# Performance work log

Hardware: AMD Instinct MI355X
Metric: run time of the kernel (lower is better)

## Reference

```python
import jax, jax.numpy as jnp
import numpy as np

MARGIN = 0.2
EPS = 1e-8
N, D_EMB, N_CLASSES = 8192, 256, 512


def setup_inputs() -> dict:
    key = jax.random.key(0)
    k1, k2 = jax.random.split(key)
    embeddings = jax.random.normal(k1, (N, D_EMB), dtype=jnp.float32)
    labels = jax.random.randint(k2, (N,), 0, N_CLASSES, dtype=jnp.int64)
    return {"embeddings": embeddings, "labels": labels}


def reference(embeddings, labels):
    # OnlineTripleLoss.forward with sampling_strategy='fixed_semi_hard', cosine metric.
    n = embeddings.shape[0]
    norms = jnp.linalg.norm(embeddings, axis=1, keepdims=True)
    xn = embeddings / jnp.maximum(norms, EPS)
    dist = 1.0 - xn @ xn.T                       # [N, N] cosine distance

    same = labels[:, None] == labels[None, :]    # same-label mask
    neg_mask = ~same
    has_neg = jnp.any(neg_mask, axis=1)          # anchor has at least one negative

    # fixed_semi_hard argmax(ap+margin-an) == argmin(an); fallback is also argmin(an)
    BIG = jnp.float32(1e9)
    dmin_neg = jnp.min(jnp.where(neg_mask, dist, BIG), axis=1)  # [N]

    # all anchor-positive combinations: same label, a < p (itertools.combinations order)
    upper = jnp.triu(jnp.ones((n, n), dtype=bool), 1)
    pair_mask = same & upper & has_neg[:, None]

    losses = jnp.maximum(dist - dmin_neg[:, None] + MARGIN, 0.0)
    count = jnp.sum(pair_mask)
    loss_sum = jnp.sum(jnp.where(pair_mask, losses, 0.0))
    loss = jnp.where(count > 0, loss_sum / jnp.maximum(count, 1).astype(jnp.float32), 0.0)
    return loss, count
```

## Files before the change

### kernel.cpp

```cpp
#include <hip/hip_runtime.h>
#include <hip/hip_bf16.h>

#define NROWS 8192
#define DEMB 256
#define MARGIN 0.2f
#define NCLS 512
#define TPC 8
#define NSTEP 16
#define MCAP 64
#define SROW 264

typedef __attribute__((ext_vector_type(4))) float f32x4;
typedef __attribute__((ext_vector_type(8))) short bf16x8;

static __device__ __forceinline__ unsigned short f2b(float f) {
    unsigned u = __builtin_bit_cast(unsigned, f);
    u += 0x7fffu + ((u >> 16) & 1u);
    return (unsigned short)(u >> 16);
}
static __device__ __forceinline__ float b2f(unsigned short b) {
    unsigned u = ((unsigned)b) << 16;
    return __builtin_bit_cast(float, u);
}
static __device__ __forceinline__ unsigned encf(float f) {
    unsigned u = __builtin_bit_cast(unsigned, f);
    return (u & 0x80000000u) ? ~u : (u | 0x80000000u);
}
static __device__ __forceinline__ float decf(unsigned e) {
    unsigned u = (e & 0x80000000u) ? (e ^ 0x80000000u) : ~e;
    return __builtin_bit_cast(float, u);
}
static __device__ __forceinline__ void gload16(const void* g, void* l) {
    __builtin_amdgcn_global_load_lds(
        (const __attribute__((address_space(1))) unsigned int*)g,
        (__attribute__((address_space(3))) unsigned int*)l, 16, 0, 0);
}

__global__ __launch_bounds__(256) void k_norm(const float* __restrict__ x,
                                              unsigned short* __restrict__ xnb,
                                              unsigned* __restrict__ amax,
                                              int* __restrict__ bcnt) {
    int gid = blockIdx.x * blockDim.x + threadIdx.x;
    if (gid < NROWS) amax[gid] = 0u;
    if (gid < NCLS) bcnt[gid] = 0;
    int row  = gid >> 6;
    int lane = threadIdx.x & 63;
    const float4* p = reinterpret_cast<const float4*>(x + (size_t)row * DEMB) + lane;
    float4 v = *p;
    float s = v.x * v.x + v.y * v.y + v.z * v.z + v.w * v.w;
#pragma unroll
    for (int m = 1; m < 64; m <<= 1) s += __shfl_xor(s, m);
    float inv = 1.0f / fmaxf(sqrtf(s), 1e-8f);
    ushort4 o;
    o.x = f2b(v.x * inv); o.y = f2b(v.y * inv);
    o.z = f2b(v.z * inv); o.w = f2b(v.w * inv);
    *(reinterpret_cast<ushort4*>(xnb + (size_t)row * DEMB) + lane) = o;
}

__global__ __launch_bounds__(256) void k_bucket(const int* __restrict__ labels,
                                                int* __restrict__ bcnt,
                                                int* __restrict__ mem) {
    int i = blockIdx.x * 256 + threadIdx.x;
    if (i < NROWS) {
        int l = labels[i];
        int slot = atomicAdd(&bcnt[l], 1);
        if (slot < MCAP) mem[l * MCAP + slot] = i;
    }
}

__global__ __launch_bounds__(512, 2) void k_maxneg(const unsigned short* __restrict__ xnb,
                                                   const int* __restrict__ labels,
                                                   unsigned* __restrict__ amax) {
    extern __shared__ char lds[];
    unsigned short* Bl = (unsigned short*)lds;

    int tid  = threadIdx.x;
    int wid  = tid >> 6, lane = tid & 63;
    int wr   = wid >> 1, wc = wid & 1;
    int arow = lane & 15, kgrp = lane >> 4;

    int i0 = blockIdx.x * 128;
    int j0 = blockIdx.y * (TPC * 128);

    bf16x8 a[2][8];
    const unsigned short* ap0 = xnb + (size_t)(i0 + wr * 32 + arow) * DEMB + kgrp * 8;
#pragma unroll
    for (int m = 0; m < 2; ++m)
#pragma unroll
        for (int kk = 0; kk < 8; ++kk)
            a[m][kk] = *(const bf16x8*)(ap0 + m * 16 * DEMB + kk * 32);

    int rlab[2][4];
#pragma unroll
    for (int m = 0; m < 2; ++m)
#pragma unroll
        for (int r = 0; r < 4; ++r)
            rlab[m][r] = labels[i0 + wr * 32 + m * 16 + kgrp * 4 + r];

    float rmax[2][4] = {{-1e30f, -1e30f, -1e30f, -1e30f},
                        {-1e30f, -1e30f, -1e30f, -1e30f}};
    f32x4 acc[2][4] = {};

    auto stage = [&](int buf, int t, int h) {
#pragma unroll
        for (int is = 0; is < 4; ++is) {
            int idx  = is * 512 + tid;
            int row  = idx >> 4;
            int colb = (idx & 15) << 4;
            int scol = (colb ^ ((row & 15) << 4)) >> 1;
            const unsigned short* src =
                xnb + (size_t)(j0 + t * 128 + row) * DEMB + h * 128 + scol;
            unsigned short* dst = Bl + buf * 16384 + is * 4096 + wid * 512;
            gload16(src, dst);
        }
    };

    int clab[4], nlab[4];
    stage(0, 0, 0);
#pragma unroll
    for (int n = 0; n < 4; ++n) clab[n] = labels[j0 + wc * 64 + n * 16 + arow];

    int sw = arow << 4;
    for (int s = 0; s < NSTEP; ++s) {
        __syncthreads();
        if (s + 1 < NSTEP) stage((s + 1) & 1, (s + 1) >> 1, (s + 1) & 1);
        int tile = s >> 1, h = s & 1;
        if (h == 0 && tile + 1 < TPC) {
#pragma unroll
            for (int n = 0; n < 4; ++n)
                nlab[n] = labels[j0 + (tile + 1) * 128 + wc * 64 + n * 16 + arow];
        }
        const char* Bt = (const char*)(Bl + (s & 1) * 16384);
        bf16x8 b[4][4];
#pragma unroll
        for (int n = 0; n < 4; ++n) {
            int rb = (wc * 64 + n * 16 + arow) * 256;
#pragma unroll
            for (int ksl = 0; ksl < 4; ++ksl)
                b[n][ksl] = *(const bf16x8*)(Bt + rb + ((ksl * 64 + kgrp * 16) ^ sw));
        }
#pragma unroll
        for (int m = 0; m < 2; ++m)
#pragma unroll
            for (int n = 0; n < 4; ++n)
#pragma unroll
                for (int ksl = 0; ksl < 4; ++ksl)
                    acc[m][n] = __builtin_amdgcn_mfma_f32_16x16x32_bf16(
                        a[m][h * 4 + ksl], b[n][ksl], acc[m][n], 0, 0, 0);
        if (h == 1) {
#pragma unroll
            for (int m = 0; m < 2; ++m)
#pragma unroll
                for (int r = 0; r < 4; ++r) {
                    float v = rmax[m][r];
                    int rl = rlab[m][r];
#pragma unroll
                    for (int n = 0; n < 4; ++n)
                        if (clab[n] != rl) v = fmaxf(v, acc[m][n][r]);
                    rmax[m][r] = v;
                }
#pragma unroll
            for (int m = 0; m < 2; ++m)
#pragma unroll
                for (int n = 0; n < 4; ++n) acc[m][n] = (f32x4){0.f, 0.f, 0.f, 0.f};
#pragma unroll
            for (int n = 0; n < 4; ++n) clab[n] = nlab[n];
        }
    }

    float* smax = (float*)Bl;
#pragma unroll
    for (int m = 0; m < 2; ++m)
#pragma unroll
        for (int r = 0; r < 4; ++r) {
            float v = rmax[m][r];
#pragma unroll
            for (int msk = 1; msk < 16; msk <<= 1) v = fmaxf(v, __shfl_xor(v, msk));
            if (arow == 0) smax[wc * 128 + wr * 32 + m * 16 + kgrp * 4 + r] = v;
        }
    __syncthreads();
    if (tid < 128) {
        float v = fmaxf(smax[tid], smax[128 + tid]);
        if (v > -1e29f) atomicMax(amax + i0 + tid, encf(v));
    }
}

__global__ __launch_bounds__(256) void k_cpairs2(const unsigned short* __restrict__ xnb,
                                                 const unsigned* __restrict__ amax,
                                                 const int* __restrict__ bcnt,
                                                 const int* __restrict__ mem,
                                                 float* __restrict__ closs,
                                                 int* __restrict__ ccnt) {
    __shared__ unsigned short srows[MCAP * SROW];
    __shared__ int mlist[MCAP];
    __shared__ float sdm[MCAP];
    __shared__ unsigned char shn[MCAP];
    __shared__ float slloss[16];
    __shared__ int slcnt[16];

    int c   = blockIdx.x;
    int tid = threadIdx.x;
    int nc  = bcnt[c];
    if (nc > MCAP) nc = MCAP;

    if (tid < nc) {
        int gi = mem[c * MCAP + tid];
        mlist[tid] = gi;
        unsigned e = amax[gi];
        shn[tid] = (e != 0u);
        sdm[tid] = 1.0f - decf(e);
    }
    __syncthreads();
    int nch = nc * 32;
    for (int ch = tid; ch < nch; ch += 256) {
        int r = ch >> 5, cc = ch & 31;
        *(bf16x8*)(srows + r * SROW + cc * 8) =
            *(const bf16x8*)(xnb + (size_t)mlist[r] * DEMB + cc * 8);
    }
    __syncthreads();

    int slot = tid >> 4, gl = tid & 15;
    int npairs = nc * (nc - 1) / 2;
    float gloss = 0.f;
    int gcnt = 0;
    for (int p = slot; p < npairs; p += 16) {
        int i = 0, rem = p;
        while (rem >= nc - 1 - i) { rem -= nc - 1 - i; ++i; }
        int j = i + 1 + rem;
        bf16x8 a0 = *(const bf16x8*)(srows + i * SROW + gl * 16);
        bf16x8 a1 = *(const bf16x8*)(srows + i * SROW + gl * 16 + 8);
        bf16x8 b0 = *(const bf16x8*)(srows + j * SROW + gl * 16);
        bf16x8 b1 = *(const bf16x8*)(srows + j * SROW + gl * 16 + 8);
        float dot = 0.f;
#pragma unroll
        for (int e = 0; e < 8; ++e) {
            dot += b2f((unsigned short)a0[e]) * b2f((unsigned short)b0[e]);
            dot += b2f((unsigned short)a1[e]) * b2f((unsigned short)b1[e]);
        }
#pragma unroll
        for (int msk = 1; msk < 16; msk <<= 1) dot += __shfl_xor(dot, msk);
        if (gl == 0) {
            int ai = (mlist[i] < mlist[j]) ? i : j;
            if (shn[ai]) {
                gloss += fmaxf(1.0f - dot - sdm[ai] + MARGIN, 0.0f);
                gcnt += 1;
            }
        }
    }
    if (gl == 0) { slloss[slot] = gloss; slcnt[slot] = gcnt; }
    __syncthreads();
    if (tid == 0) {
        float s = 0.f; int k = 0;
        for (int q = 0; q < 16; ++q) { s += slloss[q]; k += slcnt[q]; }
        closs[c] = s; ccnt[c] = k;
    }
}

__global__ __launch_bounds__(256) void k_final(const float* __restrict__ closs,
                                               const int* __restrict__ ccnt,
                                               float* __restrict__ out) {
    __shared__ float sl[256];
    __shared__ int   sc[256];
    int tid = threadIdx.x;
    float s = closs[tid] + closs[tid + 256];
    int   k = ccnt[tid] + ccnt[tid + 256];
    sl[tid] = s; sc[tid] = k;
    __syncthreads();
    for (int st = 128; st > 0; st >>= 1) {
        if (tid < st) {
            sl[tid] += sl[tid + st];
            sc[tid] += sc[tid + st];
        }
        __syncthreads();
    }
    if (tid == 0) {
        out[0] = (sc[0] > 0) ? sl[0] / (float)sc[0] : 0.0f;
        out[1] = (float)sc[0];
    }
}

extern "C" void kernel_launch(void* const* d_in, const int* in_sizes, int n_in,
                              void* d_out, int out_size, void* d_ws, size_t ws_size,
                              hipStream_t stream) {
    const float* emb  = (const float*)d_in[0];
    const int* labels = (const int*)d_in[1];
    float* out = (float*)d_out;

    char* ws = (char*)d_ws;
    unsigned short* xnb = (unsigned short*)ws;
    unsigned* amax = (unsigned*)(ws + (size_t)4 * 1024 * 1024);
    int* bcnt = (int*)(ws + (size_t)4 * 1024 * 1024 + 32768);
    int* mem  = (int*)(ws + (size_t)4 * 1024 * 1024 + 34816);
    float* closs = (float*)(ws + (size_t)4 * 1024 * 1024 + 34816 + 131072);
    int*   ccnt  = (int*)  (ws + (size_t)4 * 1024 * 1024 + 34816 + 131072 + 2048);

    k_norm<<<NROWS / 4, 256, 0, stream>>>(emb, xnb, amax, bcnt);
    k_bucket<<<NROWS / 256, 256, 0, stream>>>(labels, bcnt, mem);
    dim3 g2(NROWS / 128, NCLS / 64);
    k_maxneg<<<g2, 512, 65536, stream>>>(xnb, labels, amax);
    k_cpairs2<<<NCLS, 256, 0, stream>>>(xnb, amax, bcnt, mem, closs, ccnt);
    k_final<<<1, 256, 0, stream>>>(closs, ccnt, out);
}
```

Before: 80.13 us.

## Deepen maxneg LDS pipeline, fuse bucketing into norm, fold final reduce into pairs

The max-negative GEMM kernel now stages 64-wide K slices into a 4-deep ring buffer, using explicit vmcnt waits and raw barriers, MFMA priority boosts and a lighter XOR swizzle. This is meant to hide global-load latency better, and launch bounds now ask for higher occupancy. Label bucketing moves into the normalization kernel, and the separate final reduction kernel is replaced by global atomics with a last-block-done finalize, cutting two launches. The trade-offs are a memset launch, atomic contention, and the risk that the 64KB LDS allocation blocks the requested occupancy.

```diff
diff --git a/kernel.cpp b/kernel.cpp
--- a/kernel.cpp
+++ b/kernel.cpp
@@ -6,7 +6,7 @@
 #define MARGIN 0.2f
 #define NCLS 512
 #define TPC 8
-#define NSTEP 16
+#define NSTEP 32
 #define MCAP 64
 #define SROW 264
 
@@ -37,12 +37,18 @@
 }
 
 __global__ __launch_bounds__(256) void k_norm(const float* __restrict__ x,
+                                              const int* __restrict__ labels,
                                               unsigned short* __restrict__ xnb,
                                               unsigned* __restrict__ amax,
-                                              int* __restrict__ bcnt) {
+                                              int* __restrict__ bcnt,
+                                              int* __restrict__ mem) {
     int gid = blockIdx.x * blockDim.x + threadIdx.x;
-    if (gid < NROWS) amax[gid] = 0u;
-    if (gid < NCLS) bcnt[gid] = 0;
+    if (gid < NROWS) {
+        amax[gid] = 0u;
+        int l = labels[gid];
+        int slot = atomicAdd(&bcnt[l], 1);
+        if (slot < MCAP) mem[l * MCAP + slot] = gid;
+    }
     int row  = gid >> 6;
     int lane = threadIdx.x & 63;
     const float4* p = reinterpret_cast<const float4*>(x + (size_t)row * DEMB) + lane;
@@ -57,22 +63,12 @@
     *(reinterpret_cast<ushort4*>(xnb + (size_t)row * DEMB) + lane) = o;
 }
 
-__global__ __launch_bounds__(256) void k_bucket(const int* __restrict__ labels,
-                                                int* __restrict__ bcnt,
-                                                int* __restrict__ mem) {
-    int i = blockIdx.x * 256 + threadIdx.x;
-    if (i < NROWS) {
-        int l = labels[i];
-        int slot = atomicAdd(&bcnt[l], 1);
-        if (slot < MCAP) mem[l * MCAP + slot] = i;
-    }
-}
-
-__global__ __launch_bounds__(512, 2) void k_maxneg(const unsigned short* __restrict__ xnb,
+__global__ __launch_bounds__(512, 4) void k_maxneg(const unsigned short* __restrict__ xnb,
                                                    const int* __restrict__ labels,
                                                    unsigned* __restrict__ amax) {
     extern __shared__ char lds[];
     unsigned short* Bl = (unsigned short*)lds;
+    const char* BlC = (const char*)lds;
 
     int tid  = threadIdx.x;
     int wid  = tid >> 6, lane = tid & 63;
@@ -97,57 +93,70 @@
         for (int r = 0; r < 4; ++r)
             rlab[m][r] = labels[i0 + wr * 32 + m * 16 + kgrp * 4 + r];
 
+    int row0  = tid >> 3;
+    int colb0 = (tid & 7) << 4;
+    int scol0 = (colb0 ^ ((row0 & 7) << 4)) >> 1;
+    const unsigned short* sb = xnb + (size_t)(j0 + row0) * DEMB + scol0;
+    unsigned short* db = Bl + wid * 512;
+
+    int sx  = (arow & 7) << 4;
+    int rb0 = (wc * 64 + arow) * 128;
+    int rc0 = rb0 + ((kgrp * 16) ^ sx);
+    int rc1 = rb0 + ((64 + kgrp * 16) ^ sx);
+
     float rmax[2][4] = {{-1e30f, -1e30f, -1e30f, -1e30f},
                         {-1e30f, -1e30f, -1e30f, -1e30f}};
     f32x4 acc[2][4] = {};
-
-    auto stage = [&](int buf, int t, int h) {
-#pragma unroll
-        for (int is = 0; is < 4; ++is) {
-            int idx  = is * 512 + tid;
-            int row  = idx >> 4;
-            int colb = (idx & 15) << 4;
-            int scol = (colb ^ ((row & 15) << 4)) >> 1;
-            const unsigned short* src =
-                xnb + (size_t)(j0 + t * 128 + row) * DEMB + h * 128 + scol;
-            unsigned short* dst = Bl + buf * 16384 + is * 4096 + wid * 512;
-            gload16(src, dst);
-        }
-    };
-
     int clab[4], nlab[4];
-    stage(0, 0, 0);
 #pragma unroll
     for (int n = 0; n < 4; ++n) clab[n] = labels[j0 + wc * 64 + n * 16 + arow];
 
-    int sw = arow << 4;
+#define STAGE(S) { \
+        const unsigned short* s_ = sb + ((S) >> 2) * 32768 + ((S) & 3) * 64; \
+        unsigned short* d_ = db + ((S) & 3) * 8192; \
+        gload16(s_, d_); \
+        gload16(s_ + 16384, d_ + 4096); }
+
+    STAGE(0) STAGE(1) STAGE(2)
+
+#pragma unroll
     for (int s = 0; s < NSTEP; ++s) {
-        __syncthreads();
-        if (s + 1 < NSTEP) stage((s + 1) & 1, (s + 1) >> 1, (s + 1) & 1);
-        int tile = s >> 1, h = s & 1;
-        if (h == 0 && tile + 1 < TPC) {
+        if (s + 3 < NSTEP) STAGE(s + 3)
+        if ((s & 3) == 0 && (s >> 2) + 1 < TPC) {
 #pragma unroll
             for (int n = 0; n < 4; ++n)
-                nlab[n] = labels[j0 + (tile + 1) * 128 + wc * 64 + n * 16 + arow];
-        }
-        const char* Bt = (const char*)(Bl + (s & 1) * 16384);
-        bf16x8 b[4][4];
-#pragma unroll
-        for (int n = 0; n < 4; ++n) {
-            int rb = (wc * 64 + n * 16 + arow) * 256;
-#pragma unroll
-            for (int ksl = 0; ksl < 4; ++ksl)
-                b[n][ksl] = *(const bf16x8*)(Bt + rb + ((ksl * 64 + kgrp * 16) ^ sw));
-        }
-#pragma unroll
-        for (int m = 0; m < 2; ++m)
-#pragma unroll
-            for (int n = 0; n < 4; ++n)
-#pragma unroll
-                for (int ksl = 0; ksl < 4; ++ksl)
+                nlab[n] = labels[j0 + ((s >> 2) + 1) * 128 + wc * 64 + n * 16 + arow];
+        }
+        if (s < NSTEP - 3)      asm volatile("s_waitcnt vmcnt(6)" ::: "memory");
+        else if (s == NSTEP - 3) asm volatile("s_waitcnt vmcnt(4)" ::: "memory");
+        else if (s == NSTEP - 2) asm volatile("s_waitcnt vmcnt(2)" ::: "memory");
+        else                     asm volatile("s_waitcnt vmcnt(0)" ::: "memory");
+        __builtin_amdgcn_sched_barrier(0);
+        __builtin_amdgcn_s_barrier();
+        __builtin_amdgcn_sched_barrier(0);
+        {
+            const char* Bt = BlC + (s & 3) * 16384;
+            bf16x8 b[4][2];
+#pragma unroll
+            for (int n = 0; n < 4; ++n) {
+                b[n][0] = *(const bf16x8*)(Bt + n * 2048 + rc0);
+                b[n][1] = *(const bf16x8*)(Bt + n * 2048 + rc1);
+            }
+            __builtin_amdgcn_s_setprio(1);
+#pragma unroll
+            for (int m = 0; m < 2; ++m)
+#pragma unroll
+                for (int n = 0; n < 4; ++n) {
                     acc[m][n] = __builtin_amdgcn_mfma_f32_16x16x32_bf16(
-                        a[m][h * 4 + ksl], b[n][ksl], acc[m][n], 0, 0, 0);
-        if (h == 1) {
+                        a[m][(s & 3) * 2], b[n][0], acc[m][n], 0, 0, 0);
+                    acc[m][n] = __builtin_amdgcn_mfma_f32_16x16x32_bf16(
+                        a[m][(s & 3) * 2 + 1], b[n][1], acc[m][n], 0, 0, 0);
+                }
+            __builtin_amdgcn_s_setprio(0);
+        }
+        __builtin_amdgcn_sched_barrier(0);
+        __builtin_amdgcn_s_barrier();
+        if ((s & 3) == 3) {
 #pragma unroll
             for (int m = 0; m < 2; ++m)
 #pragma unroll
@@ -167,6 +176,7 @@
             for (int n = 0; n < 4; ++n) clab[n] = nlab[n];
         }
     }
+#undef STAGE
 
     float* smax = (float*)Bl;
 #pragma unroll
@@ -189,8 +199,10 @@
                                                  const unsigned* __restrict__ amax,
                                                  const int* __restrict__ bcnt,
                                                  const int* __restrict__ mem,
-                                                 float* __restrict__ closs,
-                                                 int* __restrict__ ccnt) {
+                                                 float* __restrict__ gsum,
+                                                 int* __restrict__ gcnt,
+                                                 unsigned* __restrict__ done,
+                                                 float* __restrict__ out) {
     __shared__ unsigned short srows[MCAP * SROW];
     __shared__ int mlist[MCAP];
     __shared__ float sdm[MCAP];
@@ -222,7 +234,7 @@
     int slot = tid >> 4, gl = tid & 15;
     int npairs = nc * (nc - 1) / 2;
     float gloss = 0.f;
-    int gcnt = 0;
+    int gc = 0;
     for (int p = slot; p < npairs; p += 16) {
         int i = 0, rem = p;
         while (rem >= nc - 1 - i) { rem -= nc - 1 - i; ++i; }
@@ -243,39 +255,25 @@
             int ai = (mlist[i] < mlist[j]) ? i : j;
             if (shn[ai]) {
                 gloss += fmaxf(1.0f - dot - sdm[ai] + MARGIN, 0.0f);
-                gcnt += 1;
+                gc += 1;
             }
         }
     }
-    if (gl == 0) { slloss[slot] = gloss; slcnt[slot] = gcnt; }
+    if (gl == 0) { slloss[slot] = gloss; slcnt[slot] = gc; }
     __syncthreads();
     if (tid == 0) {
         float s = 0.f; int k = 0;
         for (int q = 0; q < 16; ++q) { s += slloss[q]; k += slcnt[q]; }
-        closs[c] = s; ccnt[c] = k;
-    }
-}
-
-__global__ __launch_bounds__(256) void k_final(const float* __restrict__ closs,
-                                               const int* __restrict__ ccnt,
-                                               float* __restrict__ out) {
-    __shared__ float sl[256];
-    __shared__ int   sc[256];
-    int tid = threadIdx.x;
-    float s = closs[tid] + closs[tid + 256];
-    int   k = ccnt[tid] + ccnt[tid + 256];
-    sl[tid] = s; sc[tid] = k;
-    __syncthreads();
-    for (int st = 128; st > 0; st >>= 1) {
-        if (tid < st) {
-            sl[tid] += sl[tid + st];
-            sc[tid] += sc[tid + st];
-        }
-        __syncthreads();
-    }
-    if (tid == 0) {
-        out[0] = (sc[0] > 0) ? sl[0] / (float)sc[0] : 0.0f;
-        out[1] = (float)sc[0];
+        atomicAdd(gsum, s);
+        atomicAdd(gcnt, k);
+        __threadfence();
+        unsigned old = atomicAdd(done, 1u);
+        if (old == NCLS - 1) {
+            float S = atomicAdd(gsum, 0.0f);
+            int   K = atomicAdd(gcnt, 0);
+            out[0] = (K > 0) ? S / (float)K : 0.0f;
+            out[1] = (float)K;
+        }
     }
 }
 
@@ -289,15 +287,15 @@
     char* ws = (char*)d_ws;
     unsigned short* xnb = (unsigned short*)ws;
     unsigned* amax = (unsigned*)(ws + (size_t)4 * 1024 * 1024);
-    int* bcnt = (int*)(ws + (size_t)4 * 1024 * 1024 + 32768);
-    int* mem  = (int*)(ws + (size_t)4 * 1024 * 1024 + 34816);
-    float* closs = (float*)(ws + (size_t)4 * 1024 * 1024 + 34816 + 131072);
-    int*   ccnt  = (int*)  (ws + (size_t)4 * 1024 * 1024 + 34816 + 131072 + 2048);
-
-    k_norm<<<NROWS / 4, 256, 0, stream>>>(emb, xnb, amax, bcnt);
-    k_bucket<<<NROWS / 256, 256, 0, stream>>>(labels, bcnt, mem);
+    int*      bcnt = (int*)     (ws + (size_t)4 * 1024 * 1024 + 32768);
+    float*    gsum = (float*)   (ws + (size_t)4 * 1024 * 1024 + 34816);
+    int*      gcnt = (int*)     (ws + (size_t)4 * 1024 * 1024 + 34820);
+    unsigned* done = (unsigned*)(ws + (size_t)4 * 1024 * 1024 + 34824);
+    int*      mem  = (int*)     (ws + (size_t)4 * 1024 * 1024 + 36864);
+
+    hipMemsetAsync(bcnt, 0, 2048 + 16, stream);
+    k_norm<<<NROWS / 4, 256, 0, stream>>>(emb, labels, xnb, amax, bcnt, mem);
     dim3 g2(NROWS / 128, NCLS / 64);
     k_maxneg<<<g2, 512, 65536, stream>>>(xnb, labels, amax);
-    k_cpairs2<<<NCLS, 256, 0, stream>>>(xnb, amax, bcnt, mem, closs, ccnt);
-    k_final<<<1, 256, 0, stream>>>(closs, ccnt, out);
-}
+    k_cpairs2<<<NCLS, 256, 0, stream>>>(xnb, amax, bcnt, mem, gsum, gcnt, done, out);
+}
```

Result: slower. 230.4 us (+187.5%).
